# Optimization experiments

Measured on AMD Instinct MI355X. Metric: run time of the kernel, lower is better.

The kernel has to match this reference:

```python
import jax, jax.numpy as jnp
import numpy as np

T1 = -0.075410217
T2 = 0.0
T3 = 0.062207676


def my_squash2(s_j):
    # s_j: [B, 1, C, O, 1]; piecewise-linear rescale based on sorted channel-0 magnitudes.
    B, _, C, O, _ = s_j.shape
    f = s_j[:, 0, :, 0, 0]                      # [B, C] first element of each capsule
    order = jnp.argsort(f, axis=1)
    srt = jnp.take_along_axis(f, order, axis=1)  # ascending sort per sample
    i1 = jnp.sum(srt < T1, axis=1, keepdims=True)
    i2 = jnp.sum(srt < T2, axis=1, keepdims=True)
    i3 = jnp.sum(srt < T3, axis=1, keepdims=True)
    pos = jnp.arange(C)[None, :]
    seg1 = -0.074520095 * srt + 0.349297946
    seg2 = -0.534473989 * srt + 0.27196494
    seg3 = 0.637642944 * srt + 0.295330779
    seg4 = 0.169344703 * srt + 0.353784456
    # faithful to torch slices [0:i1-1], [i1:i2-1], [i2:i3-1], [i3:9] (segment-end indices untouched)
    m1 = (i1 > 0) & (pos < i1 - 1)
    m2 = (i2 > 0) & (i2 > i1) & (pos >= i1) & (pos < i2 - 1)
    m3 = (i3 > 0) & (i3 > i2) & (pos >= i2) & (pos < i3 - 1)
    m4 = (i3 < C) & (pos >= i3) & (pos < C - 1)
    new_srt = jnp.where(m1, seg1, jnp.where(m2, seg2, jnp.where(m3, seg3, jnp.where(m4, seg4, srt))))
    inv = jnp.argsort(order, axis=1)
    new_f = jnp.take_along_axis(new_srt, inv, axis=1)  # unsort back to capsule order
    # torch code mutates s_j in place: channel 0 of each capsule becomes new_f
    s_mut = s_j.at[:, 0, :, 0, 0].set(new_f)
    scale = new_f[:, None, :, None, None]            # expanded over out_channels
    return scale * s_mut, s_mut


def setup_inputs() -> dict:
    key = jax.random.key(0)
    k0, k1, k2, k3 = jax.random.split(key, 4)
    B, R, C, O, I = 100, 1152, 10, 16, 8
    return {
        "x0": jax.random.normal(k0, (B, R, I), dtype=jnp.float32),
        "x1": jax.random.normal(k1, (B, R, I), dtype=jnp.float32),
        "x2": jax.random.normal(k2, (B, 1, 28, 28), dtype=jnp.float32),
        "W": jax.random.normal(k3, (1, R, C, O, I), dtype=jnp.float32),
        "train_or_test": 0,
        "epch": 0,
    }


def reference(x0, x1, x2, W, train_or_test, epch):
    B, R, I = x0.shape
    C, O = W.shape[2], W.shape[3]
    squashed_u = jnp.broadcast_to(x0[:, :, None, :, None], (B, R, C, I, 1))
    # u_hat[b,r,c,o] = sum_i W[0,r,c,o,i] * x0[b,r,i]
    u_hat = jnp.einsum('rcoi,bri->brco', W[0], x0)[..., None]  # [B,R,C,O,1]
    b_ij = jnp.zeros((1, R, C, 1), dtype=x0.dtype)
    num_iterations = 3
    for it in range(num_iterations):
        c_ij = jax.nn.softmax(b_ij, axis=1)                    # over routes
        c_full = jnp.broadcast_to(c_ij, (B, R, C, 1))[..., None]
        s_j = jnp.sum(c_full * u_hat, axis=1, keepdims=True)   # [B,1,C,O,1]
        v_j, s_mut = my_squash2(s_j)
        if it < num_iterations - 1:
            a = jnp.einsum('brco,bco->brc', u_hat[..., 0], v_j[:, 0, :, :, 0])
            b_ij = b_ij + jnp.mean(a, axis=0)[None, :, :, None]
    Wb = jnp.broadcast_to(W, (B,) + W.shape[1:])
    return (v_j[:, 0], c_full, Wb, squashed_u, x1, x2, s_mut[:, 0])
```

## Files before the change

kernel.cpp:

```cpp
#include <hip/hip_runtime.h>

#define B 100
#define R 1152
#define C 10
#define O 16
#define I 8
#define RI 9216
#define CO 160
#define RCHUNK 32
#define NRC 36
#define KCH (RCHUNK*I)

#define WS_BCOL 0
#define WS_CSM  11520
#define WS_XT   23040
#define WS_PART 944768
#define WS_V    1520768
#define WS_SMUT 1536768

__global__ void k_init(const float* __restrict__ x0, float* __restrict__ ws) {
    int idx = blockIdx.x * 256 + threadIdx.x;
    if (idx < RI * B) {
        int k = idx / B;
        int b = idx - k * B;
        ws[WS_XT + idx] = x0[b * RI + k];
    }
    if (idx < R * C) ws[WS_BCOL + idx] = 0.f;
}

__global__ __launch_bounds__(256) void k_gemm1(const float* __restrict__ Wg,
                                               float* __restrict__ ws) {
    const int rc = blockIdx.x, c = blockIdx.y;
    const int t = threadIdx.x;
    const int r0 = rc * RCHUNK;
    __shared__ float red[256];
    __shared__ float cw[RCHUNK];
    __shared__ float lw[KCH * O];
    const float* bcol = ws + WS_BCOL + c * R;

    float lm = -3.4e38f;
    for (int r = t; r < R; r += 256) lm = fmaxf(lm, bcol[r]);
    red[t] = lm; __syncthreads();
    for (int s = 128; s > 0; s >>= 1) { if (t < s) red[t] = fmaxf(red[t], red[t + s]); __syncthreads(); }
    const float m = red[0]; __syncthreads();
    float ls = 0.f;
    for (int r = t; r < R; r += 256) ls += expf(bcol[r] - m);
    red[t] = ls; __syncthreads();
    for (int s = 128; s > 0; s >>= 1) { if (t < s) red[t] += red[t + s]; __syncthreads(); }
    const float sinv = 1.f / red[0];
    if (t < RCHUNK) {
        float w_ = expf(bcol[r0 + t] - m) * sinv;
        cw[t] = w_;
        ws[WS_CSM + (r0 + t) * C + c] = w_;
    }
    __syncthreads();

    for (int j = t; j < KCH * O; j += 256) {
        int rr = j >> 7;
        int rem = j & 127;
        int o = rem >> 3, i = rem & 7;
        lw[(rr * I + i) * O + o] = cw[rr] * Wg[((size_t)(r0 + rr) * C + c) * (O * I) + rem];
    }
    __syncthreads();

    const int bl = t & 63, og = t >> 6;
    const float* xT = ws + WS_XT + (r0 * I) * B + bl;
    const float4* lw4 = (const float4*)lw;
    float4 a0 = {0, 0, 0, 0}, a1 = {0, 0, 0, 0};
    #pragma unroll 8
    for (int k = 0; k < KCH; k++) {
        float xv0 = xT[0];
        float xv1 = xT[64];
        float4 wv = lw4[k * 4 + og];
        a0.x += xv0 * wv.x; a0.y += xv0 * wv.y; a0.z += xv0 * wv.z; a0.w += xv0 * wv.w;
        a1.x += xv1 * wv.x; a1.y += xv1 * wv.y; a1.z += xv1 * wv.z; a1.w += xv1 * wv.w;
        xT += B;
    }
    float4* part4 = (float4*)(ws + WS_PART);
    int base = ((c * NRC + rc) * B + bl) * 4 + og;
    part4[base] = a0;
    if (bl < B - 64) part4[base + 64 * 4] = a1;
}

__global__ __launch_bounds__(256) void k_squash(float* __restrict__ ws) {
    const int b = blockIdx.x, t = threadIdx.x;
    __shared__ float sl[CO];
    __shared__ float nf[C];
    if (t < CO) {
        int c = t >> 4, o = t & 15;
        float s = 0.f;
        const float* p = ws + WS_PART + ((size_t)c * NRC * B + b) * 16 + o;
        #pragma unroll
        for (int rc = 0; rc < NRC; rc++) s += p[(size_t)rc * B * 16];
        sl[t] = s;
    }
    __syncthreads();
    if (t < C) {
        float fv[C];
        #pragma unroll
        for (int c2 = 0; c2 < C; c2++) fv[c2] = sl[c2 * O];
        float mine = sl[t * O];
        int rank = 0, i1 = 0, i2 = 0, i3 = 0;
        #pragma unroll
        for (int c2 = 0; c2 < C; c2++) {
            rank += (fv[c2] < mine) || (fv[c2] == mine && c2 < t);
            i1 += fv[c2] < -0.075410217f;
            i2 += fv[c2] < 0.0f;
            i3 += fv[c2] < 0.062207676f;
        }
        float nv = mine;
        if (i1 > 0 && rank < i1 - 1)                               nv = -0.074520095f * mine + 0.349297946f;
        else if (i2 > 0 && i2 > i1 && rank >= i1 && rank < i2 - 1) nv = -0.534473989f * mine + 0.27196494f;
        else if (i3 > 0 && i3 > i2 && rank >= i2 && rank < i3 - 1) nv = 0.637642944f * mine + 0.295330779f;
        else if (i3 < C && rank >= i3 && rank < C - 1)             nv = 0.169344703f * mine + 0.353784456f;
        nf[t] = nv;
    }
    __syncthreads();
    if (t < CO) {
        int c = t >> 4, o = t & 15;
        float sv = sl[t];
        float nfv = nf[c];
        float smut = (o == 0) ? nfv : sv;
        ws[WS_SMUT + b * CO + t] = smut;
        ws[WS_V + b * CO + t] = nfv * smut;
    }
}

__global__ __launch_bounds__(256) void k_agree(const float* __restrict__ Wg,
                                               float* __restrict__ ws) {
    const int r = blockIdx.x, t = threadIdx.x;
    __shared__ float vt[32 * B];
    __shared__ float xs[I * B];
    __shared__ float arr[CO * I];
    for (int j = t; j < I * B; j += 256) xs[j] = ws[WS_XT + (size_t)r * I * B + j];
    const int i = t & 7, co0 = t >> 3;
    const float4* xs4 = (const float4*)(xs + i * B);
    const float4* vt4 = (const float4*)(vt + co0 * B);
    for (int ch = 0; ch < 5; ch++) {
        __syncthreads();
        for (int j = t; j < 32 * B; j += 256) {
            int b = j >> 5, cc = j & 31;
            vt[cc * B + b] = ws[WS_V + b * CO + ch * 32 + cc];
        }
        __syncthreads();
        float q = 0.f;
        #pragma unroll
        for (int b4 = 0; b4 < B / 4; b4++) {
            float4 xv = xs4[b4];
            float4 vv = vt4[b4];
            q += xv.x * vv.x + xv.y * vv.y + xv.z * vv.z + xv.w * vv.w;
        }
        int co = ch * 32 + co0;
        arr[co * I + i] = q * Wg[(size_t)r * (C * O * I) + co * I + i];
    }
    __syncthreads();
    if (t < C) {
        const float4* a4 = (const float4*)(arr + t * 128);
        float d = 0.f;
        #pragma unroll
        for (int m2 = 0; m2 < 32; m2++) { float4 v4 = a4[m2]; d += v4.x + v4.y + v4.z + v4.w; }
        ws[WS_BCOL + t * R + r] += d * (1.0f / B);
    }
}

__global__ void k_wb(const float* __restrict__ Wg, float4* __restrict__ out) {
    int idx = blockIdx.x * 256 + threadIdx.x;
    float4 v = ((const float4*)Wg)[idx];
    float4* dst = out + 292000 + idx;
    #pragma unroll 4
    for (int b = 0; b < B; b++) { *dst = v; dst += 368640; }
}

__global__ void k_out(const float* __restrict__ x0, const float* __restrict__ x1,
                      const float* __restrict__ x2, const float* __restrict__ ws,
                      float4* __restrict__ out) {
    const float4* x04 = (const float4*)x0;
    const float4* x14 = (const float4*)x1;
    const float4* x24 = (const float4*)x2;
    const float4* v4  = (const float4*)(ws + WS_V);
    const float4* sm4 = (const float4*)(ws + WS_SMUT);
    const float4* cs4 = (const float4*)(ws + WS_CSM);
    const int stride = gridDim.x * blockDim.x;
    for (int u = blockIdx.x * blockDim.x + threadIdx.x; u < 2850000; u += stride) {
        int g = (u < 292000) ? u : u + 36864000;
        float4 val;
        if (g >= 37156000 && g < 39460000) {
            int j = g - 37156000;
            int br = j / 20;
            val = x04[br * 2 + (j & 1)];
        } else if (g >= 4000 && g < 292000) {
            int j = g - 4000;
            val = cs4[j % 2880];
        } else if (g < 4000) {
            val = v4[g];
        } else if (g < 39690400) {
            val = x14[g - 39460000];
        } else if (g < 39710000) {
            val = x24[g - 39690400];
        } else {
            val = sm4[g - 39710000];
        }
        out[g] = val;
    }
}

extern "C" void kernel_launch(void* const* d_in, const int* in_sizes, int n_in,
                              void* d_out, int out_size, void* d_ws, size_t ws_size,
                              hipStream_t stream) {
    (void)in_sizes; (void)n_in; (void)out_size; (void)ws_size;
    const float* x0 = (const float*)d_in[0];
    const float* x1 = (const float*)d_in[1];
    const float* x2 = (const float*)d_in[2];
    const float* Wg = (const float*)d_in[3];
    float* ws = (float*)d_ws;
    float4* out = (float4*)d_out;

    hipLaunchKernelGGL(k_init, dim3(3600), dim3(256), 0, stream, x0, ws);
    for (int it = 0; it < 3; it++) {
        hipLaunchKernelGGL(k_gemm1, dim3(NRC, C), dim3(256), 0, stream, Wg, ws);
        hipLaunchKernelGGL(k_squash, dim3(B), dim3(256), 0, stream, ws);
        if (it < 2)
            hipLaunchKernelGGL(k_agree, dim3(R), dim3(256), 0, stream, Wg, ws);
    }
    hipLaunchKernelGGL(k_wb, dim3(1440), dim3(256), 0, stream, Wg, out);
    hipLaunchKernelGGL(k_out, dim3(2048), dim3(256), 0, stream, x0, x1, x2, ws, out);
}
```

Before: 245.7 us.

## Spread broadcast-W output writes across compute kernels with nontemporal stores

Removes the standalone k_wb kernel and splits the 147MB broadcast of W into 7200 work units. These are appended as extra blocks to k_init, each gemm/squash/agree launch and k_out, so the memory-bound writes overlap with the latency-bound routing kernels. Output stores now use nontemporal stores to avoid polluting cache. The trade-off is more complex grid indexing and possible contention slowing the critical-path compute blocks.

```diff
diff --git a/kernel.cpp b/kernel.cpp
--- a/kernel.cpp
+++ b/kernel.cpp
@@ -11,6 +11,11 @@
 #define NRC 36
 #define KCH (RCHUNK*I)
 
+typedef float f4raw __attribute__((ext_vector_type(4)));
+__device__ __forceinline__ void nt_store4(const float4& v, float4* p) {
+    __builtin_nontemporal_store(*(const f4raw*)&v, (f4raw*)p);
+}
+
 #define WS_BCOL 0
 #define WS_CSM  11520
 #define WS_XT   23040
@@ -18,7 +23,29 @@
 #define WS_V    1520768
 #define WS_SMUT 1536768
 
-__global__ void k_init(const float* __restrict__ x0, float* __restrict__ ws) {
+#define WB_OUT_BASE 292000
+#define WB_WSTRIDE  368640
+#define WB_NCHUNK   1440
+#define WB_BG       20
+#define WB_UNITS    7200
+
+__device__ __forceinline__ void wb_unit(const float4* __restrict__ W4,
+                                        float4* __restrict__ out, int unit) {
+    int wchunk = unit % WB_NCHUNK;
+    int bg = unit / WB_NCHUNK;
+    int idx = wchunk * 256 + threadIdx.x;
+    float4 v = W4[idx];
+    float4* dst = out + WB_OUT_BASE + (size_t)bg * WB_BG * WB_WSTRIDE + idx;
+    #pragma unroll
+    for (int b = 0; b < WB_BG; b++) {
+        nt_store4(v, dst);
+        dst += WB_WSTRIDE;
+    }
+}
+
+__global__ void k_init(const float* __restrict__ x0, float* __restrict__ ws,
+                       const float4* __restrict__ W4, float4* __restrict__ out) {
+    if (blockIdx.x >= 3600) { wb_unit(W4, out, 0 + (blockIdx.x - 3600)); return; }
     int idx = blockIdx.x * 256 + threadIdx.x;
     if (idx < RI * B) {
         int k = idx / B;
@@ -29,7 +56,12 @@
 }
 
 __global__ __launch_bounds__(256) void k_gemm1(const float* __restrict__ Wg,
-                                               float* __restrict__ ws) {
+                                               float* __restrict__ ws,
+                                               float4* __restrict__ out, int wbBase) {
+    if (blockIdx.x >= NRC) {
+        wb_unit((const float4*)Wg, out, wbBase + (blockIdx.x - NRC) + 90 * blockIdx.y);
+        return;
+    }
     const int rc = blockIdx.x, c = blockIdx.y;
     const int t = threadIdx.x;
     const int r0 = rc * RCHUNK;
@@ -82,7 +114,10 @@
     if (bl < B - 64) part4[base + 64 * 4] = a1;
 }
 
-__global__ __launch_bounds__(256) void k_squash(float* __restrict__ ws) {
+__global__ __launch_bounds__(256) void k_squash(float* __restrict__ ws,
+                                                const float4* __restrict__ W4,
+                                                float4* __restrict__ out, int wbBase) {
+    if (blockIdx.x >= B) { wb_unit(W4, out, wbBase + (blockIdx.x - B)); return; }
     const int b = blockIdx.x, t = threadIdx.x;
     __shared__ float sl[CO];
     __shared__ float nf[C];
@@ -127,7 +162,9 @@
 }
 
 __global__ __launch_bounds__(256) void k_agree(const float* __restrict__ Wg,
-                                               float* __restrict__ ws) {
+                                               float* __restrict__ ws,
+                                               float4* __restrict__ out, int wbBase) {
+    if (blockIdx.x >= R) { wb_unit((const float4*)Wg, out, wbBase + (blockIdx.x - R)); return; }
     const int r = blockIdx.x, t = threadIdx.x;
     __shared__ float vt[32 * B];
     __shared__ float xs[I * B];
@@ -163,25 +200,20 @@
     }
 }
 
-__global__ void k_wb(const float* __restrict__ Wg, float4* __restrict__ out) {
-    int idx = blockIdx.x * 256 + threadIdx.x;
-    float4 v = ((const float4*)Wg)[idx];
-    float4* dst = out + 292000 + idx;
-    #pragma unroll 4
-    for (int b = 0; b < B; b++) { *dst = v; dst += 368640; }
-}
-
+#define KOUT_BLOCKS 2048
 __global__ void k_out(const float* __restrict__ x0, const float* __restrict__ x1,
                       const float* __restrict__ x2, const float* __restrict__ ws,
-                      float4* __restrict__ out) {
+                      const float4* __restrict__ W4, float4* __restrict__ out,
+                      int wbBase) {
+    if (blockIdx.x >= KOUT_BLOCKS) { wb_unit(W4, out, wbBase + (blockIdx.x - KOUT_BLOCKS)); return; }
     const float4* x04 = (const float4*)x0;
     const float4* x14 = (const float4*)x1;
     const float4* x24 = (const float4*)x2;
     const float4* v4  = (const float4*)(ws + WS_V);
     const float4* sm4 = (const float4*)(ws + WS_SMUT);
     const float4* cs4 = (const float4*)(ws + WS_CSM);
-    const int stride = gridDim.x * blockDim.x;
-    for (int u = blockIdx.x * blockDim.x + threadIdx.x; u < 2850000; u += stride) {
+    const int stride = KOUT_BLOCKS * 256;
+    for (int u = blockIdx.x * 256 + threadIdx.x; u < 2850000; u += stride) {
         int g = (u < 292000) ? u : u + 36864000;
         float4 val;
         if (g >= 37156000 && g < 39460000) {
@@ -200,7 +232,7 @@
         } else {
             val = sm4[g - 39710000];
         }
-        out[g] = val;
+        nt_store4(val, &out[g]);
     }
 }
 
@@ -212,16 +244,20 @@
     const float* x1 = (const float*)d_in[1];
     const float* x2 = (const float*)d_in[2];
     const float* Wg = (const float*)d_in[3];
+    const float4* W4 = (const float4*)Wg;
     float* ws = (float*)d_ws;
     float4* out = (float4*)d_out;
 
-    hipLaunchKernelGGL(k_init, dim3(3600), dim3(256), 0, stream, x0, ws);
+    hipLaunchKernelGGL(k_init, dim3(3600 + 600), dim3(256), 0, stream, x0, ws, W4, out);
     for (int it = 0; it < 3; it++) {
-        hipLaunchKernelGGL(k_gemm1, dim3(NRC, C), dim3(256), 0, stream, Wg, ws);
-        hipLaunchKernelGGL(k_squash, dim3(B), dim3(256), 0, stream, ws);
+        hipLaunchKernelGGL(k_gemm1, dim3(NRC + 90, C), dim3(256), 0, stream,
+                           Wg, ws, out, 600 + 900 * it);
+        hipLaunchKernelGGL(k_squash, dim3(B + 500), dim3(256), 0, stream,
+                           ws, W4, out, 3300 + 500 * it);
         if (it < 2)
-            hipLaunchKernelGGL(k_agree, dim3(R), dim3(256), 0, stream, Wg, ws);
-    }
-    hipLaunchKernelGGL(k_wb, dim3(1440), dim3(256), 0, stream, Wg, out);
-    hipLaunchKernelGGL(k_out, dim3(2048), dim3(256), 0, stream, x0, x1, x2, ws, out);
-}
+            hipLaunchKernelGGL(k_agree, dim3(R + 700), dim3(256), 0, stream,
+                               Wg, ws, out, 4800 + 700 * it);
+    }
+    hipLaunchKernelGGL(k_out, dim3(KOUT_BLOCKS + 1000), dim3(256), 0, stream,
+                       x0, x1, x2, ws, W4, out, 6200);
+}
```

Result: faster. 234.8 us (-4.4%).

## Overlap output streaming copies with routing kernels and drop transpose init

Applied to the files above, without the earlier changes.

The large output copies (broadcast W, squashed_u, x1, x2) are split into work units and handed to extra blocks appended to each routing kernel launch, so the memory-bound copies run alongside the small compute kernels instead of after them. The separate x0 transpose kernel is removed: the GEMM transposes x0 tiles through shared memory, and the agreement kernel reads x0 directly. The first iteration skips the softmax because the weights are uniform, and the route coefficients are written only in the last iteration. The chunk size is halved to get more GEMM blocks, and output writes use nontemporal stores. This adds complex unit-indexing bookkeeping and contention between copy blocks and compute blocks.

```diff
diff --git a/kernel.cpp b/kernel.cpp
--- a/kernel.cpp
+++ b/kernel.cpp
@@ -6,52 +6,113 @@
 #define O 16
 #define I 8
 #define RI 9216
-#define CO 160
-#define RCHUNK 32
-#define NRC 36
-#define KCH (RCHUNK*I)
+#define RC2 2304
+#define RCHUNK 16
+#define NRC 72
+#define KCH 128
+
+#define T1c (-0.075410217f)
+#define T3c (0.062207676f)
+
+typedef float f4raw __attribute__((ext_vector_type(4)));
+static __device__ __forceinline__ void nt_store4(const float4& v, float4* p) {
+    __builtin_nontemporal_store(*(const f4raw*)&v, (f4raw*)p);
+}
 
 #define WS_BCOL 0
 #define WS_CSM  11520
-#define WS_XT   23040
-#define WS_PART 944768
-#define WS_V    1520768
-#define WS_SMUT 1536768
-
-__global__ void k_init(const float* __restrict__ x0, float* __restrict__ ws) {
-    int idx = blockIdx.x * 256 + threadIdx.x;
-    if (idx < RI * B) {
-        int k = idx / B;
-        int b = idx - k * B;
-        ws[WS_XT + idx] = x0[b * RI + k];
-    }
-    if (idx < R * C) ws[WS_BCOL + idx] = 0.f;
-}
-
-__global__ __launch_bounds__(256) void k_gemm1(const float* __restrict__ Wg,
-                                               float* __restrict__ ws) {
-    const int rc = blockIdx.x, c = blockIdx.y;
+#define WS_PART 23040
+#define WS_VOB  1175040
+#define WS_VBCO 1191040
+#define WS_SMUT 1207040
+
+#define O_VJ 0
+#define O_CF 4000
+#define O_WB 292000
+#define O_SQ 37156000
+#define O_X1 39460000
+#define O_X2 39690400
+#define O_SM 39710000
+
+#define U_WB 7200
+#define U_SQ 563
+#define U_X1 57
+#define U_X2 5
+#define U_TOT 7825
+
+__device__ void stream_unit(int u, const float4* __restrict__ W4,
+                            const float4* __restrict__ x04,
+                            const float4* __restrict__ x14,
+                            const float4* __restrict__ x24,
+                            float4* __restrict__ out) {
     const int t = threadIdx.x;
+    if (u < U_WB) {
+        int wchunk = u % 1440, bg = u / 1440;
+        int idx = wchunk * 256 + t;
+        float4 v = W4[idx];
+        float4* dst = out + O_WB + (size_t)bg * 20 * 368640 + idx;
+        #pragma unroll
+        for (int b = 0; b < 20; b++) { nt_store4(v, dst); dst += 368640; }
+    } else if (u < U_WB + U_SQ) {
+        int s = u - U_WB;
+        int m0 = s * 4096, m1 = m0 + 4096; if (m1 > 2304000) m1 = 2304000;
+        for (int m = m0 + t; m < m1; m += 256) {
+            float4 v = x04[(m / 20) * 2 + (m & 1)];
+            nt_store4(v, &out[O_SQ + m]);
+        }
+    } else if (u < U_WB + U_SQ + U_X1) {
+        int s = u - U_WB - U_SQ;
+        int m0 = s * 4096, m1 = m0 + 4096; if (m1 > 230400) m1 = 230400;
+        for (int m = m0 + t; m < m1; m += 256) nt_store4(x14[m], &out[O_X1 + m]);
+    } else {
+        int s = u - U_WB - U_SQ - U_X1;
+        int m0 = s * 4096, m1 = m0 + 4096; if (m1 > 19600) m1 = 19600;
+        for (int m = m0 + t; m < m1; m += 256) nt_store4(x24[m], &out[O_X2 + m]);
+    }
+}
+
+__global__ __launch_bounds__(256) void k_gemm(const float* __restrict__ Wg,
+                                              const float* __restrict__ x0,
+                                              float* __restrict__ ws,
+                                              const float4* __restrict__ x14,
+                                              const float4* __restrict__ x24,
+                                              float4* __restrict__ out,
+                                              int it, int ubase) {
+    const int t = threadIdx.x;
+    const float4* x04 = (const float4*)x0;
+    if (blockIdx.x >= 720) {
+        int k = blockIdx.x - 720;
+        #pragma unroll 1
+        for (int n = 0; n < 3; n++)
+            stream_unit(ubase + k * 3 + n, (const float4*)Wg, x04, x14, x24, out);
+        return;
+    }
+    const int rc = blockIdx.x % NRC, c = blockIdx.x / NRC;
     const int r0 = rc * RCHUNK;
     __shared__ float red[256];
     __shared__ float cw[RCHUNK];
-    __shared__ float lw[KCH * O];
-    const float* bcol = ws + WS_BCOL + c * R;
-
-    float lm = -3.4e38f;
-    for (int r = t; r < R; r += 256) lm = fmaxf(lm, bcol[r]);
-    red[t] = lm; __syncthreads();
-    for (int s = 128; s > 0; s >>= 1) { if (t < s) red[t] = fmaxf(red[t], red[t + s]); __syncthreads(); }
-    const float m = red[0]; __syncthreads();
-    float ls = 0.f;
-    for (int r = t; r < R; r += 256) ls += expf(bcol[r] - m);
-    red[t] = ls; __syncthreads();
-    for (int s = 128; s > 0; s >>= 1) { if (t < s) red[t] += red[t + s]; __syncthreads(); }
-    const float sinv = 1.f / red[0];
-    if (t < RCHUNK) {
-        float w_ = expf(bcol[r0 + t] - m) * sinv;
-        cw[t] = w_;
-        ws[WS_CSM + (r0 + t) * C + c] = w_;
+    __shared__ __align__(16) float lw[KCH * O];
+    __shared__ float tp[64][104];
+
+    if (it > 0) {
+        const float* bcol = ws + WS_BCOL + c * R;
+        float lm = -3.4e38f;
+        for (int r = t; r < R; r += 256) lm = fmaxf(lm, bcol[r]);
+        red[t] = lm; __syncthreads();
+        for (int s = 128; s > 0; s >>= 1) { if (t < s) red[t] = fmaxf(red[t], red[t + s]); __syncthreads(); }
+        const float m = red[0]; __syncthreads();
+        float ls = 0.f;
+        for (int r = t; r < R; r += 256) ls += expf(bcol[r] - m);
+        red[t] = ls; __syncthreads();
+        for (int s = 128; s > 0; s >>= 1) { if (t < s) red[t] += red[t + s]; __syncthreads(); }
+        const float sinv = 1.f / red[0];
+        if (t < RCHUNK) cw[t] = expf(bcol[r0 + t] - m) * sinv;
+        if (it == 2 && rc == 0) {
+            for (int r = t; r < R; r += 256)
+                ws[WS_CSM + r * C + c] = expf(bcol[r] - m) * sinv;
+        }
+    } else {
+        if (t < RCHUNK) cw[t] = 1.0f / 1152.0f;
     }
     __syncthreads();
 
@@ -59,39 +120,62 @@
         int rr = j >> 7;
         int rem = j & 127;
         int o = rem >> 3, i = rem & 7;
-        lw[(rr * I + i) * O + o] = cw[rr] * Wg[((size_t)(r0 + rr) * C + c) * (O * I) + rem];
-    }
-    __syncthreads();
+        lw[((rr * I + i) << 4) + o] = cw[rr] * Wg[((size_t)(r0 + rr) * C + c) * 128 + rem];
+    }
 
     const int bl = t & 63, og = t >> 6;
-    const float* xT = ws + WS_XT + (r0 * I) * B + bl;
-    const float4* lw4 = (const float4*)lw;
+    int b2 = bl + 64; if (b2 > 103) b2 = 103;
     float4 a0 = {0, 0, 0, 0}, a1 = {0, 0, 0, 0};
-    #pragma unroll 8
-    for (int k = 0; k < KCH; k++) {
-        float xv0 = xT[0];
-        float xv1 = xT[64];
-        float4 wv = lw4[k * 4 + og];
-        a0.x += xv0 * wv.x; a0.y += xv0 * wv.y; a0.z += xv0 * wv.z; a0.w += xv0 * wv.w;
-        a1.x += xv1 * wv.x; a1.y += xv1 * wv.y; a1.z += xv1 * wv.z; a1.w += xv1 * wv.w;
-        xT += B;
+    for (int p = 0; p < 2; p++) {
+        __syncthreads();
+        int colbase = r0 * 2 + p * 16;
+        for (int e = t; e < 1600; e += 256) {
+            int b = e >> 4, q = e & 15;
+            float4 v = x04[(size_t)b * RC2 + colbase + q];
+            tp[q * 4 + 0][b] = v.x; tp[q * 4 + 1][b] = v.y;
+            tp[q * 4 + 2][b] = v.z; tp[q * 4 + 3][b] = v.w;
+        }
+        tp[t >> 2][100 + (t & 3)] = 0.f;
+        __syncthreads();
+        const float4* lwp = (const float4*)lw + p * 64 * 4;
+        #pragma unroll 8
+        for (int k = 0; k < 64; k++) {
+            float xv0 = tp[k][bl];
+            float xv1 = tp[k][b2];
+            float4 wv = lwp[k * 4 + og];
+            a0.x += xv0 * wv.x; a0.y += xv0 * wv.y; a0.z += xv0 * wv.z; a0.w += xv0 * wv.w;
+            a1.x += xv1 * wv.x; a1.y += xv1 * wv.y; a1.z += xv1 * wv.z; a1.w += xv1 * wv.w;
+        }
     }
     float4* part4 = (float4*)(ws + WS_PART);
     int base = ((c * NRC + rc) * B + bl) * 4 + og;
     part4[base] = a0;
-    if (bl < B - 64) part4[base + 64 * 4] = a1;
-}
-
-__global__ __launch_bounds__(256) void k_squash(float* __restrict__ ws) {
-    const int b = blockIdx.x, t = threadIdx.x;
-    __shared__ float sl[CO];
+    if (bl < 36) part4[base + 64 * 4] = a1;
+}
+
+__global__ __launch_bounds__(256) void k_squash(float* __restrict__ ws,
+                                                const float* __restrict__ Wg,
+                                                const float* __restrict__ x0,
+                                                const float4* __restrict__ x14,
+                                                const float4* __restrict__ x24,
+                                                float4* __restrict__ out, int ubase) {
+    const int t = threadIdx.x;
+    if (blockIdx.x >= B) {
+        int k = blockIdx.x - B;
+        #pragma unroll 1
+        for (int n = 0; n < 2; n++)
+            stream_unit(ubase + k * 2 + n, (const float4*)Wg, (const float4*)x0, x14, x24, out);
+        return;
+    }
+    const int b = blockIdx.x;
+    __shared__ float sl[160];
     __shared__ float nf[C];
-    if (t < CO) {
+    if (t < 160) {
         int c = t >> 4, o = t & 15;
         float s = 0.f;
         const float* p = ws + WS_PART + ((size_t)c * NRC * B + b) * 16 + o;
-        #pragma unroll
-        for (int rc = 0; rc < NRC; rc++) s += p[(size_t)rc * B * 16];
+        #pragma unroll 8
+        for (int rc = 0; rc < NRC; rc++) s += p[rc * 1600];
         sl[t] = s;
     }
     __syncthreads();
@@ -104,9 +188,9 @@
         #pragma unroll
         for (int c2 = 0; c2 < C; c2++) {
             rank += (fv[c2] < mine) || (fv[c2] == mine && c2 < t);
-            i1 += fv[c2] < -0.075410217f;
+            i1 += fv[c2] < T1c;
             i2 += fv[c2] < 0.0f;
-            i3 += fv[c2] < 0.062207676f;
+            i3 += fv[c2] < T3c;
         }
         float nv = mine;
         if (i1 > 0 && rank < i1 - 1)                               nv = -0.074520095f * mine + 0.349297946f;
@@ -116,42 +200,60 @@
         nf[t] = nv;
     }
     __syncthreads();
-    if (t < CO) {
+    if (t < 160) {
         int c = t >> 4, o = t & 15;
         float sv = sl[t];
         float nfv = nf[c];
         float smut = (o == 0) ? nfv : sv;
-        ws[WS_SMUT + b * CO + t] = smut;
-        ws[WS_V + b * CO + t] = nfv * smut;
+        float v = nfv * smut;
+        ws[WS_VBCO + b * 160 + t] = v;
+        ws[WS_SMUT + b * 160 + t] = smut;
+        ws[WS_VOB + t * B + b] = v;
     }
 }
 
 __global__ __launch_bounds__(256) void k_agree(const float* __restrict__ Wg,
-                                               float* __restrict__ ws) {
-    const int r = blockIdx.x, t = threadIdx.x;
-    __shared__ float vt[32 * B];
-    __shared__ float xs[I * B];
-    __shared__ float arr[CO * I];
-    for (int j = t; j < I * B; j += 256) xs[j] = ws[WS_XT + (size_t)r * I * B + j];
+                                               const float* __restrict__ x0,
+                                               float* __restrict__ ws,
+                                               const float4* __restrict__ x14,
+                                               const float4* __restrict__ x24,
+                                               float4* __restrict__ out,
+                                               int it, int ubase) {
+    const int t = threadIdx.x;
+    if (blockIdx.x >= R) {
+        int k = blockIdx.x - R;
+        #pragma unroll 1
+        for (int n = 0; n < 3; n++)
+            stream_unit(ubase + k * 3 + n, (const float4*)Wg, (const float4*)x0, x14, x24, out);
+        return;
+    }
+    const int r = blockIdx.x;
+    __shared__ __align__(16) float vt[3200];
+    __shared__ __align__(16) float xs[800];
+    __shared__ __align__(16) float arr[1280];
+    const float4* x04 = (const float4*)x0;
+    if (t < 200) {
+        int b = t >> 1, half = t & 1;
+        float4 v = x04[(size_t)b * RC2 + r * 2 + half];
+        xs[(half * 4 + 0) * B + b] = v.x; xs[(half * 4 + 1) * B + b] = v.y;
+        xs[(half * 4 + 2) * B + b] = v.z; xs[(half * 4 + 3) * B + b] = v.w;
+    }
     const int i = t & 7, co0 = t >> 3;
     const float4* xs4 = (const float4*)(xs + i * B);
     const float4* vt4 = (const float4*)(vt + co0 * B);
     for (int ch = 0; ch < 5; ch++) {
         __syncthreads();
-        for (int j = t; j < 32 * B; j += 256) {
-            int b = j >> 5, cc = j & 31;
-            vt[cc * B + b] = ws[WS_V + b * CO + ch * 32 + cc];
-        }
+        for (int j = t; j < 3200; j += 256) vt[j] = ws[WS_VOB + ch * 3200 + j];
         __syncthreads();
         float q = 0.f;
         #pragma unroll
-        for (int b4 = 0; b4 < B / 4; b4++) {
+        for (int b4 = 0; b4 < 25; b4++) {
             float4 xv = xs4[b4];
             float4 vv = vt4[b4];
             q += xv.x * vv.x + xv.y * vv.y + xv.z * vv.z + xv.w * vv.w;
         }
         int co = ch * 32 + co0;
-        arr[co * I + i] = q * Wg[(size_t)r * (C * O * I) + co * I + i];
+        arr[co * I + i] = q * Wg[(size_t)r * 1280 + co * I + i];
     }
     __syncthreads();
     if (t < C) {
@@ -159,49 +261,32 @@
         float d = 0.f;
         #pragma unroll
         for (int m2 = 0; m2 < 32; m2++) { float4 v4 = a4[m2]; d += v4.x + v4.y + v4.z + v4.w; }
-        ws[WS_BCOL + t * R + r] += d * (1.0f / B);
-    }
-}
-
-__global__ void k_wb(const float* __restrict__ Wg, float4* __restrict__ out) {
-    int idx = blockIdx.x * 256 + threadIdx.x;
-    float4 v = ((const float4*)Wg)[idx];
-    float4* dst = out + 292000 + idx;
-    #pragma unroll 4
-    for (int b = 0; b < B; b++) { *dst = v; dst += 368640; }
-}
-
-__global__ void k_out(const float* __restrict__ x0, const float* __restrict__ x1,
-                      const float* __restrict__ x2, const float* __restrict__ ws,
-                      float4* __restrict__ out) {
-    const float4* x04 = (const float4*)x0;
-    const float4* x14 = (const float4*)x1;
-    const float4* x24 = (const float4*)x2;
-    const float4* v4  = (const float4*)(ws + WS_V);
+        float* dst = ws + WS_BCOL + t * R + r;
+        float val = d * (1.0f / B);
+        if (it == 0) *dst = val; else *dst += val;
+    }
+}
+
+__global__ __launch_bounds__(256) void k_out(const float* __restrict__ x0,
+                                             const float* __restrict__ x1,
+                                             const float* __restrict__ x2,
+                                             float* __restrict__ ws,
+                                             const float* __restrict__ Wg,
+                                             float4* __restrict__ out) {
+    const int bid = blockIdx.x, t = threadIdx.x;
+    const float4* cs4 = (const float4*)(ws + WS_CSM);
+    const float4* vb4 = (const float4*)(ws + WS_VBCO);
     const float4* sm4 = (const float4*)(ws + WS_SMUT);
-    const float4* cs4 = (const float4*)(ws + WS_CSM);
-    const int stride = gridDim.x * blockDim.x;
-    for (int u = blockIdx.x * blockDim.x + threadIdx.x; u < 2850000; u += stride) {
-        int g = (u < 292000) ? u : u + 36864000;
-        float4 val;
-        if (g >= 37156000 && g < 39460000) {
-            int j = g - 37156000;
-            int br = j / 20;
-            val = x04[br * 2 + (j & 1)];
-        } else if (g >= 4000 && g < 292000) {
-            int j = g - 4000;
-            val = cs4[j % 2880];
-        } else if (g < 4000) {
-            val = v4[g];
-        } else if (g < 39690400) {
-            val = x14[g - 39460000];
-        } else if (g < 39710000) {
-            val = x24[g - 39690400];
-        } else {
-            val = sm4[g - 39710000];
-        }
-        out[g] = val;
-    }
+    for (int j = bid * 256 + t; j < 296000; j += 2048 * 256) {
+        float4 v; int g;
+        if (j < 4000)        { v = vb4[j]; g = j; }
+        else if (j < 292000) { v = cs4[(j - 4000) % 2880]; g = j; }
+        else                 { v = sm4[j - 292000]; g = O_SM + (j - 292000); }
+        nt_store4(v, &out[g]);
+    }
+    if (bid < U_TOT - 6300)
+        stream_unit(6300 + bid, (const float4*)Wg, (const float4*)x0,
+                    (const float4*)x1, (const float4*)x2, out);
 }
 
 extern "C" void kernel_launch(void* const* d_in, const int* in_sizes, int n_in,
@@ -212,16 +297,18 @@
     const float* x1 = (const float*)d_in[1];
     const float* x2 = (const float*)d_in[2];
     const float* Wg = (const float*)d_in[3];
+    const float4* x14 = (const float4*)x1;
+    const float4* x24 = (const float4*)x2;
     float* ws = (float*)d_ws;
     float4* out = (float4*)d_out;
 
-    hipLaunchKernelGGL(k_init, dim3(3600), dim3(256), 0, stream, x0, ws);
-    for (int it = 0; it < 3; it++) {
-        hipLaunchKernelGGL(k_gemm1, dim3(NRC, C), dim3(256), 0, stream, Wg, ws);
-        hipLaunchKernelGGL(k_squash, dim3(B), dim3(256), 0, stream, ws);
-        if (it < 2)
-            hipLaunchKernelGGL(k_agree, dim3(R), dim3(256), 0, stream, Wg, ws);
-    }
-    hipLaunchKernelGGL(k_wb, dim3(1440), dim3(256), 0, stream, Wg, out);
-    hipLaunchKernelGGL(k_out, dim3(2048), dim3(256), 0, stream, x0, x1, x2, ws, out);
-}
+    hipLaunchKernelGGL(k_gemm,   dim3(1020), dim3(256), 0, stream, Wg, x0, ws, x14, x24, out, 0, 0);
+    hipLaunchKernelGGL(k_squash, dim3(400),  dim3(256), 0, stream, ws, Wg, x0, x14, x24, out, 900);
+    hipLaunchKernelGGL(k_agree,  dim3(1452), dim3(256), 0, stream, Wg, x0, ws, x14, x24, out, 0, 1500);
+    hipLaunchKernelGGL(k_gemm,   dim3(1020), dim3(256), 0, stream, Wg, x0, ws, x14, x24, out, 1, 2400);
+    hipLaunchKernelGGL(k_squash, dim3(400),  dim3(256), 0, stream, ws, Wg, x0, x14, x24, out, 3300);
+    hipLaunchKernelGGL(k_agree,  dim3(1452), dim3(256), 0, stream, Wg, x0, ws, x14, x24, out, 1, 3900);
+    hipLaunchKernelGGL(k_gemm,   dim3(1020), dim3(256), 0, stream, Wg, x0, ws, x14, x24, out, 2, 4800);
+    hipLaunchKernelGGL(k_squash, dim3(400),  dim3(256), 0, stream, ws, Wg, x0, x14, x24, out, 5700);
+    hipLaunchKernelGGL(k_out,    dim3(2048), dim3(256), 0, stream, x0, x1, x2, ws, Wg, out);
+}
```

After: 227.0 us. 7.6% less time.
